# Optimization experiments

Hardware: AMD Instinct MI355X
Metric: run time of the kernel (lower is better)

The kernel has to match this reference:

```python
import jax, jax.numpy as jnp
import numpy as np
from jax import lax

NX, NY = 6, 6
NB = NX * NY            # 36 blocks
B, S = 64, 256          # batch, sample_count
EPS = 1e-6

def build_edges(nx, ny):
    edges = []
    for i in range(nx):
        for j in range(ny):
            for dx, dy in [(-1, 0), (0, -1), (0, 1), (1, 0)]:
                x, y = i + dx, j + dy
                if 0 <= x < nx and 0 <= y < ny:
                    edges.append((j * nx + i, y * nx + x))
    return np.array(edges, np.int32)   # (120, 2)

EDGES_NP = build_edges(NX, NY)
NE = len(EDGES_NP)  # 120

def setup_inputs() -> dict:
    key = jax.random.key(0)
    ks = jax.random.split(key, 24)
    f32 = jnp.float32
    d = {
        "image":      jax.random.normal(ks[0], (B, 1, 32, 32), f32),
        "edge_noise": jax.random.uniform(ks[1], (B, S, NE), f32),
        "u_s":        jax.random.uniform(ks[2], (B, S, NB), f32),
        "u_d":        jax.random.uniform(ks[3], (B, S, NB), f32),
        # CNN params (OIHW)
        "cw1": jax.random.normal(ks[4], (32, 1, 5, 5), f32) * 0.05,
        "cb1": jnp.zeros((32,), f32),
        "cw2": jax.random.normal(ks[5], (32, 32, 5, 5), f32) * 0.05,
        "cb2": jnp.zeros((32,), f32),
        "cw3": jax.random.normal(ks[6], (64, 32, 5, 5), f32) * 0.05,
        "cb3": jnp.zeros((64,), f32),
        "cw4": jax.random.normal(ks[7], (64, 64, 5, 5), f32) * 0.05,
        "cb4": jnp.zeros((64,), f32),
        # is_connected MLP
        "wc1": jax.random.normal(ks[8], (256, 256), f32) * 0.05,
        "bc1": jnp.zeros((256,), f32),
        "wc2": jax.random.normal(ks[9], (256, NE), f32) * 0.05,
        "bc2": jnp.zeros((NE,), f32),
        # is_endpoint MLP
        "we1": jax.random.normal(ks[10], (256, 256), f32) * 0.05,
        "be1": jnp.zeros((256,), f32),
        "we2": jax.random.normal(ks[11], (256, NB), f32) * 0.05,
        "be2": jnp.zeros((NB,), f32),
        "edges": jnp.asarray(EDGES_NP),  # (NE, 2) int32, constants
    }
    return d

def _conv(x, w, b):
    y = lax.conv_general_dilated(x, w, (1, 1), 'VALID',
                                 dimension_numbers=('NCHW', 'OIHW', 'NCHW'))
    return y + b[None, :, None, None]

def _pool2(x):
    return lax.reduce_window(x, -jnp.inf, lax.max, (1, 1, 2, 2), (1, 1, 2, 2), 'VALID')

def reference(image, edge_noise, u_s, u_d,
              cw1, cb1, cw2, cb2, cw3, cb3, cw4, cb4,
              wc1, bc1, wc2, bc2, we1, be1, we2, be2, edges):
    # ---- CNN feature extractor ----
    h = _conv(image, cw1, cb1)
    h = _conv(h, cw2, cb2)
    h = _pool2(h)
    h = _conv(h, cw3, cb3)
    h = _conv(h, cw4, cb4)
    h = _pool2(h)
    emb = h.reshape(h.shape[0], -1)              # (B, 256)

    # ---- heads ----
    p_conn = jax.nn.sigmoid(jax.nn.relu(emb @ wc1 + bc1) @ wc2 + bc2)   # (B, NE)
    p_ep   = jax.nn.sigmoid(jax.nn.relu(emb @ we1 + be1) @ we2 + be2)   # (B, NB)

    pc = jnp.clip(p_conn, EPS, 1.0 - EPS)
    pe = jnp.clip(p_ep, EPS, 1.0 - EPS)
    cat = pe / pe.sum(-1, keepdims=True)
    logcat = jnp.log(cat)                        # (B, NB)

    # ---- Monte-Carlo sampling (ISED blackbox) ----
    conn = (edge_noise < pc[:, None, :]).astype(pc.dtype)               # (B,S,NE) Bernoulli
    g_s = -jnp.log(-jnp.log(jnp.clip(u_s, EPS, 1.0 - EPS)))
    g_d = -jnp.log(-jnp.log(jnp.clip(u_d, EPS, 1.0 - EPS)))
    s_idx = jnp.argmax(logcat[:, None, :] + g_s, axis=-1)               # (B,S) categorical
    d_idx = jnp.argmax(logcat[:, None, :] + g_d, axis=-1)               # (B,S)

    # ---- batched BFS reachability via boolean matrix squaring ----
    oh_u = jax.nn.one_hot(edges[:, 0], NB, dtype=pc.dtype)              # (NE, NB)
    oh_v = jax.nn.one_hot(edges[:, 1], NB, dtype=pc.dtype)
    e_sym = jnp.einsum('eu,ev->euv', oh_u, oh_v) + jnp.einsum('eu,ev->evu', oh_u, oh_v)
    A = jnp.minimum(jnp.einsum('bse,euv->bsuv', conn, e_sym), 1.0)      # (B,S,36,36)

    R = jnp.minimum(A + jnp.eye(NB, dtype=A.dtype), 1.0)
    for _ in range(6):                           # (I+A)^(2^6), covers path len<=36
        R = jnp.minimum(R @ R, 1.0)
    P = jnp.minimum(A @ R, 1.0)                  # paths of length >= 1 (BFS semantics)

    Pv = jnp.take_along_axis(P, s_idx[:, :, None, None], axis=2)[:, :, 0, :]  # (B,S,36)
    exists = (jnp.take_along_axis(Pv, d_idx[:, :, None], axis=2)[:, :, 0] > 0.5).astype(pc.dtype)  # (B,S)

    # ---- sample-probability weighting (differentiable ISED estimator) ----
    logw = (conn * jnp.log(pc)[:, None, :] + (1.0 - conn) * jnp.log1p(-pc)[:, None, :]).sum(-1)
    logw = logw + jnp.take_along_axis(logcat, s_idx, axis=1) \
                + jnp.take_along_axis(logcat, d_idx, axis=1)            # (B,S)
    w = jax.nn.softmax(logw, axis=1)
    p1 = (w * exists).sum(axis=1)                # P(path exists)
    return jnp.stack([1.0 - p1, p1], axis=-1)    # (B, 2)
```

## Files before the change

### kernel.cpp

```cpp
#include <hip/hip_runtime.h>

typedef unsigned long long u64;
#define EPSF 1e-6f

__global__ __launch_bounds__(1024, 4) void k_conv2(const float* __restrict__ img,
                                                   const float* __restrict__ cw1,
                                                   const float* __restrict__ cb1,
                                                   const float* __restrict__ cw2,
                                                   const float* __restrict__ cb2,
                                                   float* __restrict__ p1w) {
  int ocq = blockIdx.x, b = blockIdx.y;
  __shared__ float smem[33440];
  float* w2s = smem + 25984;
  float* simg = smem + 32384;
  int t = threadIdx.x;
  if (t < 1024) {
    int y = t >> 5, x = t & 31;
    simg[y * 33 + x] = img[b * 1024 + t];
  }
  {
    const float4* src = (const float4*)(cw2 + ocq * 8 * 800);
    for (int k4 = t; k4 < 1600; k4 += 1024) {
      float4 v = src[k4];
      float vv[4] = {v.x, v.y, v.z, v.w};
      int k = k4 * 4;
#pragma unroll
      for (int r = 0; r < 4; ++r) {
        int kk = k + r;
        int o = kk / 800, rest = kk % 800;
        w2s[rest * 8 + o] = vv[r];
      }
    }
  }
  __syncthreads();
  if (t < 896) {
    int ic = t / 28, x = t % 28;
    float w1[25];
#pragma unroll
    for (int k = 0; k < 25; ++k) w1[k] = cw1[ic * 25 + k];
    float bias = cb1[ic];
    float acc[5];
#pragma unroll
    for (int k = 0; k < 5; ++k) acc[k] = bias;
    float* orow = smem + ic * 812 + x;
#pragma unroll
    for (int rr = 0; rr < 32; ++rr) {
      float in[5];
#pragma unroll
      for (int c = 0; c < 5; ++c) in[c] = simg[rr * 33 + x + c];
#pragma unroll
      for (int ky = 0; ky < 5; ++ky) {
        if (rr < ky || rr - ky > 27) continue;
        int slot = (rr - ky) % 5;
#pragma unroll
        for (int kx = 0; kx < 5; ++kx)
          acc[slot] = fmaf(w1[ky * 5 + kx], in[kx], acc[slot]);
      }
      if (rr >= 4) {
        int slot = (rr - 4) % 5;
        orow[(rr - 4) * 29] = acc[slot];
        acc[slot] = bias;
      }
    }
  }
  int w = __builtin_amdgcn_readfirstlane(t >> 6);
  int ocg = w & 1;
  int icq = w >> 1;
  int l = t & 63;
  int py = l >> 3, px = l & 7;
  int oc0 = ocq * 8 + ocg * 4;
  float acc[4][9];
#pragma unroll
  for (int o = 0; o < 4; ++o)
#pragma unroll
    for (int e = 0; e < 9; ++e) acc[o][e] = 0.f;
  __syncthreads();

  const float* base0 = smem + icq * 4 * 812 + (3 * py) * 29 + 3 * px;
  const float* wk0 = w2s + icq * 800 + ocg * 4;
#pragma unroll
  for (int icl = 0; icl < 4; ++icl) {
    const float* base = base0 + icl * 812;
    float win[7][7];
#pragma unroll
    for (int rr = 0; rr < 7; ++rr)
#pragma unroll
      for (int m = 0; m < 7; ++m) win[rr][m] = base[rr * 29 + m];
    const float* wk = wk0 + icl * 200;
#pragma unroll
    for (int ky = 0; ky < 5; ++ky) {
      float wq[5][4];
#pragma unroll
      for (int kx = 0; kx < 5; ++kx)
        *(float4*)wq[kx] = *(const float4*)(wk + (ky * 5 + kx) * 8);
#pragma unroll
      for (int i = 0; i < 3; ++i) {
#pragma unroll
        for (int kx = 0; kx < 5; ++kx) {
#pragma unroll
          for (int jj = 0; jj < 3; ++jj) {
            float v = win[i + ky][jj + kx];
            acc[0][i * 3 + jj] = fmaf(wq[kx][0], v, acc[0][i * 3 + jj]);
            acc[1][i * 3 + jj] = fmaf(wq[kx][1], v, acc[1][i * 3 + jj]);
            acc[2][i * 3 + jj] = fmaf(wq[kx][2], v, acc[2][i * 3 + jj]);
            acc[3][i * 3 + jj] = fmaf(wq[kx][3], v, acc[3][i * 3 + jj]);
          }
        }
      }
    }
  }

  __syncthreads();
  float* slots = smem;
  float* cbuf = smem + 18432;
  int chunk = ocg * 2304 + l * 9;
  if (icq >= 4) {
    float* d = slots + (icq - 4) * 4608 + chunk;
#pragma unroll
    for (int o = 0; o < 4; ++o)
#pragma unroll
      for (int e = 0; e < 9; ++e) d[o * 576 + e] = acc[o][e];
  }
  __syncthreads();
  if (icq < 4) {
    const float* s = slots + icq * 4608 + chunk;
#pragma unroll
    for (int o = 0; o < 4; ++o)
#pragma unroll
      for (int e = 0; e < 9; ++e) acc[o][e] += s[o * 576 + e];
  }
  __syncthreads();
  if (icq == 2 || icq == 3) {
    float* d = slots + (icq - 2) * 4608 + chunk;
#pragma unroll
    for (int o = 0; o < 4; ++o)
#pragma unroll
      for (int e = 0; e < 9; ++e) d[o * 576 + e] = acc[o][e];
  }
  __syncthreads();
  if (icq < 2) {
    const float* s = slots + icq * 4608 + chunk;
#pragma unroll
    for (int o = 0; o < 4; ++o)
#pragma unroll
      for (int e = 0; e < 9; ++e) acc[o][e] += s[o * 576 + e];
  }
  __syncthreads();
  if (icq == 1) {
    float* d = slots + chunk;
#pragma unroll
    for (int o = 0; o < 4; ++o)
#pragma unroll
      for (int e = 0; e < 9; ++e) d[o * 576 + e] = acc[o][e];
  }
  __syncthreads();
  if (icq == 0) {
    const float* s = slots + chunk;
#pragma unroll
    for (int o = 0; o < 4; ++o) {
      float bias = cb2[oc0 + o];
#pragma unroll
      for (int i = 0; i < 3; ++i)
#pragma unroll
        for (int jj = 0; jj < 3; ++jj)
          cbuf[(ocg * 4 + o) * 576 + (3 * py + i) * 24 + 3 * px + jj] =
              acc[o][i * 3 + jj] + s[o * 576 + i * 3 + jj] + bias;
    }
  }
  __syncthreads();
  for (int k = t; k < 1152; k += 1024) {
    int o = k / 144, rem = k % 144;
    int PY = rem / 12, PX = rem % 12;
    const float* b0 = cbuf + o * 576 + (2 * PY) * 24 + 2 * PX;
    float m = fmaxf(fmaxf(b0[0], b0[1]), fmaxf(b0[24], b0[25]));
    p1w[((size_t)b * 32 + ocq * 8 + o) * 144 + PY * 12 + PX] = m;
  }
}

__global__ __launch_bounds__(256) void k_conv3(const float* __restrict__ p1w,
                                               const float* __restrict__ cw3,
                                               const float* __restrict__ cb3,
                                               float* __restrict__ c3) {
  int oc8 = blockIdx.x, b = blockIdx.y;
  __shared__ float smem[11008];
  float* w3s = smem;
  float* ins = smem + 6400;
  int t = threadIdx.x;
  {
    const float4* src = (const float4*)(p1w + b * 32 * 144);
    float4* dst = (float4*)ins;
    for (int k = t; k < 1152; k += 256) dst[k] = src[k];
  }
  {
    const float4* src = (const float4*)(cw3 + oc8 * 8 * 800);
    for (int k4 = t; k4 < 1600; k4 += 256) {
      float4 v = src[k4];
      float vv[4] = {v.x, v.y, v.z, v.w};
      int k = k4 * 4;
#pragma unroll
      for (int r = 0; r < 4; ++r) {
        int kk = k + r;
        int o = kk / 800, rest = kk % 800;
        w3s[rest * 8 + o] = vv[r];
      }
    }
  }
  int g = t >> 4, p = t & 15;
  int ocg = p >> 3, row = p & 7;
  float acc[4][8];
#pragma unroll
  for (int j = 0; j < 4; ++j)
#pragma unroll
    for (int c = 0; c < 8; ++c) acc[j][c] = 0.f;
  __syncthreads();
#pragma unroll
  for (int icl = 0; icl < 2; ++icl) {
    int ic = g + icl * 16;
#pragma unroll
    for (int ky = 0; ky < 5; ++ky) {
      const float4* rp = (const float4*)(ins + ic * 144 + (row + ky) * 12);
      float win[12];
#pragma unroll
      for (int q = 0; q < 3; ++q) {
        float4 v = rp[q];
        win[4 * q] = v.x; win[4 * q + 1] = v.y; win[4 * q + 2] = v.z; win[4 * q + 3] = v.w;
      }
      const float* wb = w3s + (ic * 25 + ky * 5) * 8 + ocg * 4;
#pragma unroll
      for (int kx = 0; kx < 5; ++kx) {
        float wq[4];
        *(float4*)wq = *(const float4*)(wb + kx * 8);
#pragma unroll
        for (int c = 0; c < 8; ++c) {
#pragma unroll
          for (int j = 0; j < 4; ++j) acc[j][c] = fmaf(wq[j], win[c + kx], acc[j][c]);
        }
      }
    }
  }
  float* buf = smem;
  __syncthreads();
  if (g >= 8) {
    float* d = buf + (g - 8) * 512 + p * 32;
#pragma unroll
    for (int j = 0; j < 4; ++j)
#pragma unroll
      for (int c = 0; c < 8; ++c) d[j * 8 + c] = acc[j][c];
  }
  __syncthreads();
  if (g < 8) {
    const float* s = buf + g * 512 + p * 32;
#pragma unroll
    for (int j = 0; j < 4; ++j)
#pragma unroll
      for (int c = 0; c < 8; ++c) acc[j][c] += s[j * 8 + c];
  }
  __syncthreads();
  if (g >= 4 && g < 8) {
    float* d = buf + (g - 4) * 512 + p * 32;
#pragma unroll
    for (int j = 0; j < 4; ++j)
#pragma unroll
      for (int c = 0; c < 8; ++c) d[j * 8 + c] = acc[j][c];
  }
  __syncthreads();
  if (g < 4) {
    const float* s = buf + g * 512 + p * 32;
#pragma unroll
    for (int j = 0; j < 4; ++j)
#pragma unroll
      for (int c = 0; c < 8; ++c) acc[j][c] += s[j * 8 + c];
  }
  __syncthreads();
  if (g == 2 || g == 3) {
    float* d = buf + (g - 2) * 512 + p * 32;
#pragma unroll
    for (int j = 0; j < 4; ++j)
#pragma unroll
      for (int c = 0; c < 8; ++c) d[j * 8 + c] = acc[j][c];
  }
  __syncthreads();
  if (g < 2) {
    const float* s = buf + g * 512 + p * 32;
#pragma unroll
    for (int j = 0; j < 4; ++j)
#pragma unroll
      for (int c = 0; c < 8; ++c) acc[j][c] += s[j * 8 + c];
  }
  __syncthreads();
  if (g == 1) {
    float* d = buf + p * 32;
#pragma unroll
    for (int j = 0; j < 4; ++j)
#pragma unroll
      for (int c = 0; c < 8; ++c) d[j * 8 + c] = acc[j][c];
  }
  __syncthreads();
  if (g == 0) {
    const float* s = buf + p * 32;
#pragma unroll
    for (int j = 0; j < 4; ++j) {
      float bias = cb3[oc8 * 8 + ocg * 4 + j];
      float4 v0, v1;
      v0.x = acc[j][0] + s[j * 8 + 0] + bias; v0.y = acc[j][1] + s[j * 8 + 1] + bias;
      v0.z = acc[j][2] + s[j * 8 + 2] + bias; v0.w = acc[j][3] + s[j * 8 + 3] + bias;
      v1.x = acc[j][4] + s[j * 8 + 4] + bias; v1.y = acc[j][5] + s[j * 8 + 5] + bias;
      v1.z = acc[j][6] + s[j * 8 + 6] + bias; v1.w = acc[j][7] + s[j * 8 + 7] + bias;
      float* op = c3 + (b * 64 + oc8 * 8 + ocg * 4 + j) * 64 + row * 8;
      *(float4*)op = v0; *(float4*)(op + 4) = v1;
    }
  }
}

__global__ __launch_bounds__(256) void k_conv4(const float* __restrict__ c3,
                                               const float* __restrict__ cw4,
                                               const float* __restrict__ cb4,
                                               float* __restrict__ emb) {
  int oc8 = blockIdx.x, b = blockIdx.y;
  __shared__ float smem[17152];
  float* w4s = smem;
  float* ins = smem + 12800;
  int t = threadIdx.x;
  {
    const float4* src = (const float4*)(c3 + b * 4096);
    for (int k = t; k < 1024; k += 256) {
      int ic = k >> 4, q = k & 15;
      *(float4*)(ins + ic * 68 + q * 4) = src[k];
    }
  }
  {
    const float4* src = (const float4*)(cw4 + oc8 * 8 * 1600);
    for (int k4 = t; k4 < 3200; k4 += 256) {
      float4 v = src[k4];
      float vv[4] = {v.x, v.y, v.z, v.w};
      int k = k4 * 4;
#pragma unroll
      for (int r = 0; r < 4; ++r) {
        int kk = k + r;
        int o = kk / 1600, rest = kk % 1600;
        w4s[rest * 8 + o] = vv[r];
      }
    }
  }
  int g = t >> 3, p = t & 7;
  int ocg = p >> 2, row = p & 3;
  float acc[4][4];
#pragma unroll
  for (int j = 0; j < 4; ++j)
#pragma unroll
    for (int c = 0; c < 4; ++c) acc[j][c] = 0.f;
  __syncthreads();
#pragma unroll
  for (int icl = 0; icl < 2; ++icl) {
    int ic = g + icl * 32;
#pragma unroll
    for (int ky = 0; ky < 5; ++ky) {
      const float4* rp = (const float4*)(ins + ic * 68 + (row + ky) * 8);
      float win[8];
#pragma unroll
      for (int q = 0; q < 2; ++q) {
        float4 v = rp[q];
        win[4 * q] = v.x; win[4 * q + 1] = v.y; win[4 * q + 2] = v.z; win[4 * q + 3] = v.w;
      }
      const float* wb = w4s + (ic * 25 + ky * 5) * 8 + ocg * 4;
#pragma unroll
      for (int kx = 0; kx < 5; ++kx) {
        float wq[4];
        *(float4*)wq = *(const float4*)(wb + kx * 8);
#pragma unroll
        for (int c = 0; c < 4; ++c) {
#pragma unroll
          for (int j = 0; j < 4; ++j) acc[j][c] = fmaf(wq[j], win[c + kx], acc[j][c]);
        }
      }
    }
  }
  float* buf = smem;
#pragma unroll
  for (int half = 16; half >= 1; half >>= 1) {
    __syncthreads();
    if (g >= half && g < 2 * half) {
      float* d = buf + (g - half) * 128 + p * 16;
#pragma unroll
      for (int j = 0; j < 4; ++j)
#pragma unroll
        for (int c = 0; c < 4; ++c) d[j * 4 + c] = acc[j][c];
    }
    __syncthreads();
    if (g < half) {
      const float* s = buf + g * 128 + p * 16;
#pragma unroll
      for (int j = 0; j < 4; ++j)
#pragma unroll
        for (int c = 0; c < 4; ++c) acc[j][c] += s[j * 4 + c];
    }
  }
  float* pb = buf + 2048;
  if (g == 0) {
#pragma unroll
    for (int j = 0; j < 4; ++j) {
      float bias = cb4[oc8 * 8 + ocg * 4 + j];
#pragma unroll
      for (int c = 0; c < 4; ++c) pb[(ocg * 4 + j) * 16 + row * 4 + c] = acc[j][c] + bias;
    }
  }
  __syncthreads();
  if (t < 32) {
    int o = t >> 2, q = t & 3, py = q >> 1, px = q & 1;
    const float* b0 = pb + o * 16 + (2 * py) * 4 + 2 * px;
    float m = fmaxf(fmaxf(b0[0], b0[1]), fmaxf(b0[4], b0[5]));
    emb[b * 256 + (oc8 * 8 + o) * 4 + py * 2 + px] = m;
  }
}

__global__ __launch_bounds__(256) void k_tail(const float* __restrict__ emb,
    const float* __restrict__ wc1, const float* __restrict__ bc1,
    const float* __restrict__ wc2, const float* __restrict__ bc2,
    const float* __restrict__ we1, const float* __restrict__ be1,
    const float* __restrict__ we2, const float* __restrict__ be2,
    const float* __restrict__ enoise, const float* __restrict__ us,
    const float* __restrict__ ud, const int* __restrict__ edges,
    float* __restrict__ out) {
  int b = blockIdx.x, t = threadIdx.x;
  __shared__ float e_s[256], h_s[256];
  __shared__ __align__(16) float pc_s[120];
  __shared__ __align__(16) float lpc_s[120];
  __shared__ __align__(16) float l1m_s[120];
  __shared__ __align__(16) float lcat_s[36];
  __shared__ __align__(16) int einfo[120];
  __shared__ float red_s[256];
  __shared__ float aux;
  e_s[t] = emb[b * 256 + t];
  if (t < 120) {
    int u = edges[2 * t], v = edges[2 * t + 1];
    int d = v - u;
    int isV = (d == 6 || d == -6) ? 1 : 0;
    int pos = d > 0 ? u : v;
    einfo[t] = pos | (isV << 6);
  }
  __syncthreads();
  {
    float s = bc1[t];
    for (int i = 0; i < 256; i += 4) {
      s = fmaf(e_s[i], wc1[i * 256 + t], s);
      s = fmaf(e_s[i + 1], wc1[(i + 1) * 256 + t], s);
      s = fmaf(e_s[i + 2], wc1[(i + 2) * 256 + t], s);
      s = fmaf(e_s[i + 3], wc1[(i + 3) * 256 + t], s);
    }
    h_s[t] = fmaxf(s, 0.f);
  }
  __syncthreads();
  if (t < 120) {
    float s2 = bc2[t];
    for (int i = 0; i < 256; ++i) s2 = fmaf(h_s[i], wc2[i * 120 + t], s2);
    float p = 1.f / (1.f + expf(-s2));
    p = fminf(fmaxf(p, EPSF), 1.f - EPSF);
    pc_s[t] = p;
    lpc_s[t] = logf(p);
    l1m_s[t] = log1pf(-p);
  }
  __syncthreads();
  {
    float s = be1[t];
    for (int i = 0; i < 256; i += 4) {
      s = fmaf(e_s[i], we1[i * 256 + t], s);
      s = fmaf(e_s[i + 1], we1[(i + 1) * 256 + t], s);
      s = fmaf(e_s[i + 2], we1[(i + 2) * 256 + t], s);
      s = fmaf(e_s[i + 3], we1[(i + 3) * 256 + t], s);
    }
    h_s[t] = fmaxf(s, 0.f);
  }
  __syncthreads();
  if (t < 36) {
    float s2 = be2[t];
    for (int i = 0; i < 256; ++i) s2 = fmaf(h_s[i], we2[i * 36 + t], s2);
    float p = 1.f / (1.f + expf(-s2));
    p = fminf(fmaxf(p, EPSF), 1.f - EPSF);
    red_s[t] = p;
  }
  __syncthreads();
  if (t == 0) {
    float sm = 0.f;
    for (int j = 0; j < 36; ++j) sm += red_s[j];
    aux = sm;
  }
  __syncthreads();
  if (t < 36) lcat_s[t] = logf(red_s[t] / aux);
  __syncthreads();

  float logw = 0.f;
  u64 H = 0, V = 0;
  {
    const float4* np = (const float4*)(enoise + ((size_t)(b * 256 + t)) * 120);
#pragma unroll
    for (int q = 0; q < 30; ++q) {
      float4 nz = np[q];
      float4 p4 = ((const float4*)pc_s)[q];
      float4 lp4 = ((const float4*)lpc_s)[q];
      float4 lm4 = ((const float4*)l1m_s)[q];
      int4 e4 = ((const int4*)einfo)[q];
      float nv[4] = {nz.x, nz.y, nz.z, nz.w};
      float pv[4] = {p4.x, p4.y, p4.z, p4.w};
      float lv[4] = {lp4.x, lp4.y, lp4.z, lp4.w};
      float mv[4] = {lm4.x, lm4.y, lm4.z, lm4.w};
      int ev[4] = {e4.x, e4.y, e4.z, e4.w};
#pragma unroll
      for (int r = 0; r < 4; ++r) {
        bool conn = nv[r] < pv[r];
        logw += conn ? lv[r] : mv[r];
        if (conn) {
          u64 bit = 1ull << (ev[r] & 63);
          if (ev[r] & 64) V |= bit; else H |= bit;
        }
      }
    }
  }
  int si = 0, di = 0;
  {
    const float4* up = (const float4*)(us + ((size_t)(b * 256 + t)) * 36);
    float best = -1e30f;
#pragma unroll
    for (int q = 0; q < 9; ++q) {
      float4 uv = up[q];
      float4 lc4 = ((const float4*)lcat_s)[q];
      float vv[4] = {uv.x, uv.y, uv.z, uv.w};
      float lc[4] = {lc4.x, lc4.y, lc4.z, lc4.w};
#pragma unroll
      for (int r = 0; r < 4; ++r) {
        float u = fminf(fmaxf(vv[r], EPSF), 1.f - EPSF);
        float gq = -logf(-logf(u));
        float val = lc[r] + gq;
        if (val > best) { best = val; si = q * 4 + r; }
      }
    }
  }
  {
    const float4* up = (const float4*)(ud + ((size_t)(b * 256 + t)) * 36);
    float best = -1e30f;
#pragma unroll
    for (int q = 0; q < 9; ++q) {
      float4 uv = up[q];
      float4 lc4 = ((const float4*)lcat_s)[q];
      float vv[4] = {uv.x, uv.y, uv.z, uv.w};
      float lc[4] = {lc4.x, lc4.y, lc4.z, lc4.w};
#pragma unroll
      for (int r = 0; r < 4; ++r) {
        float u = fminf(fmaxf(vv[r], EPSF), 1.f - EPSF);
        float gq = -logf(-logf(u));
        float val = lc[r] + gq;
        if (val > best) { best = val; di = q * 4 + r; }
      }
    }
  }
  logw += lcat_s[si] + lcat_s[di];

  u64 comp = 1ull << si;
  while (true) {
    u64 prev = comp;
    comp |= ((comp & H) << 1) | ((comp >> 1) & H);
    comp |= ((comp & V) << 6) | ((comp >> 6) & V);
    if (comp == prev) break;
  }
  float ex;
  if (si == di) ex = (comp != (1ull << si)) ? 1.f : 0.f;
  else ex = ((comp >> di) & 1ull) ? 1.f : 0.f;

  __syncthreads();
  red_s[t] = logw; __syncthreads();
  for (int off = 128; off > 0; off >>= 1) {
    if (t < off) red_s[t] = fmaxf(red_s[t], red_s[t + off]);
    __syncthreads();
  }
  float m = red_s[0]; __syncthreads();
  float evx = expf(logw - m);
  red_s[t] = evx; __syncthreads();
  for (int off = 128; off > 0; off >>= 1) {
    if (t < off) red_s[t] += red_s[t + off];
    __syncthreads();
  }
  float den = red_s[0]; __syncthreads();
  red_s[t] = evx * ex; __syncthreads();
  for (int off = 128; off > 0; off >>= 1) {
    if (t < off) red_s[t] += red_s[t + off];
    __syncthreads();
  }
  if (t == 0) {
    float p1v = red_s[0] / den;
    out[b * 2] = 1.f - p1v;
    out[b * 2 + 1] = p1v;
  }
}

extern "C" void kernel_launch(void* const* d_in, const int* in_sizes, int n_in,
                              void* d_out, int out_size, void* d_ws, size_t ws_size,
                              hipStream_t stream) {
  const float* image = (const float*)d_in[0];
  const float* enoise = (const float*)d_in[1];
  const float* us = (const float*)d_in[2];
  const float* udn = (const float*)d_in[3];
  const float* cw1 = (const float*)d_in[4];
  const float* cb1 = (const float*)d_in[5];
  const float* cw2 = (const float*)d_in[6];
  const float* cb2 = (const float*)d_in[7];
  const float* cw3 = (const float*)d_in[8];
  const float* cb3 = (const float*)d_in[9];
  const float* cw4 = (const float*)d_in[10];
  const float* cb4 = (const float*)d_in[11];
  const float* wc1 = (const float*)d_in[12];
  const float* bc1 = (const float*)d_in[13];
  const float* wc2 = (const float*)d_in[14];
  const float* bc2 = (const float*)d_in[15];
  const float* we1 = (const float*)d_in[16];
  const float* be1 = (const float*)d_in[17];
  const float* we2 = (const float*)d_in[18];
  const float* be2 = (const float*)d_in[19];
  const int* edges = (const int*)d_in[20];

  float* ws = (float*)d_ws;
  float* p1w = ws;
  float* c3 = ws + 294912;
  float* emb = ws + 557056;
  float* outp = (float*)d_out;

  k_conv2<<<dim3(4, 64), dim3(1024), 0, stream>>>(image, cw1, cb1, cw2, cb2, p1w);
  k_conv3<<<dim3(8, 64), dim3(256), 0, stream>>>(p1w, cw3, cb3, c3);
  k_conv4<<<dim3(8, 64), dim3(256), 0, stream>>>(c3, cw4, cb4, emb);
  k_tail<<<dim3(64), dim3(256), 0, stream>>>(emb, wc1, bc1, wc2, bc2,
                                             we1, be1, we2, be2,
                                             enoise, us, udn, edges, outp);
}
```

Measured before the change: 130.4 us.

## Split sampling tail across 4 blocks per batch with staged smem loads and finalize kernel

The tail kernel is split so each batch row runs on 4 blocks, each handling 64 samples. Noise and uniform inputs are loaded coalesced into padded shared memory, and the per-sample work runs on one wavefront that reduces with shuffles instead of block-wide shared-memory reductions. Partial max, sum and hit values are combined by a new small kernel using log-sum-exp rescaling. The trade-off is that each of the 4 blocks recomputes the two MLPs, only 64 of 256 threads do the sampling work, and there is one more kernel launch.

```diff
diff --git a/kernel.cpp b/kernel.cpp
--- a/kernel.cpp
+++ b/kernel.cpp
@@ -413,22 +413,24 @@
   }
 }
 
-__global__ __launch_bounds__(256) void k_tail(const float* __restrict__ emb,
+__global__ __launch_bounds__(256) void k_hmc(const float* __restrict__ emb,
     const float* __restrict__ wc1, const float* __restrict__ bc1,
     const float* __restrict__ wc2, const float* __restrict__ bc2,
     const float* __restrict__ we1, const float* __restrict__ be1,
     const float* __restrict__ we2, const float* __restrict__ be2,
     const float* __restrict__ enoise, const float* __restrict__ us,
     const float* __restrict__ ud, const int* __restrict__ edges,
-    float* __restrict__ out) {
-  int b = blockIdx.x, t = threadIdx.x;
-  __shared__ float e_s[256], h_s[256];
+    float* __restrict__ part3) {
+  int chunk = blockIdx.x, b = blockIdx.y, t = threadIdx.x;
+  __shared__ __align__(16) float en_s[64 * 124];
+  __shared__ __align__(16) float us_s[64 * 40];
+  __shared__ __align__(16) float ud_s[64 * 40];
+  __shared__ float e_s[256], h_s[256], pe_s[36];
   __shared__ __align__(16) float pc_s[120];
   __shared__ __align__(16) float lpc_s[120];
   __shared__ __align__(16) float l1m_s[120];
   __shared__ __align__(16) float lcat_s[36];
   __shared__ __align__(16) int einfo[120];
-  __shared__ float red_s[256];
   __shared__ float aux;
   e_s[t] = emb[b * 256 + t];
   if (t < 120) {
@@ -438,6 +440,25 @@
     int pos = d > 0 ? u : v;
     einfo[t] = pos | (isV << 6);
   }
+  {
+    const float4* src = (const float4*)(enoise + ((size_t)(b * 256 + chunk * 64)) * 120);
+    for (int k = t; k < 1920; k += 256) {
+      float4 v = src[k];
+      int s = k / 30, e4 = k % 30;
+      *(float4*)(en_s + s * 124 + e4 * 4) = v;
+    }
+  }
+  {
+    const float4* srcA = (const float4*)(us + ((size_t)(b * 256 + chunk * 64)) * 36);
+    const float4* srcB = (const float4*)(ud + ((size_t)(b * 256 + chunk * 64)) * 36);
+    for (int k = t; k < 576; k += 256) {
+      float4 va = srcA[k];
+      float4 vb = srcB[k];
+      int s = k / 9, e4 = k % 9;
+      *(float4*)(us_s + s * 40 + e4 * 4) = va;
+      *(float4*)(ud_s + s * 40 + e4 * 4) = vb;
+    }
+  }
   __syncthreads();
   {
     float s = bc1[t];
@@ -476,119 +497,127 @@
     for (int i = 0; i < 256; ++i) s2 = fmaf(h_s[i], we2[i * 36 + t], s2);
     float p = 1.f / (1.f + expf(-s2));
     p = fminf(fmaxf(p, EPSF), 1.f - EPSF);
-    red_s[t] = p;
+    pe_s[t] = p;
   }
   __syncthreads();
   if (t == 0) {
     float sm = 0.f;
-    for (int j = 0; j < 36; ++j) sm += red_s[j];
+    for (int j = 0; j < 36; ++j) sm += pe_s[j];
     aux = sm;
   }
   __syncthreads();
-  if (t < 36) lcat_s[t] = logf(red_s[t] / aux);
-  __syncthreads();
-
-  float logw = 0.f;
-  u64 H = 0, V = 0;
-  {
-    const float4* np = (const float4*)(enoise + ((size_t)(b * 256 + t)) * 120);
-#pragma unroll
-    for (int q = 0; q < 30; ++q) {
-      float4 nz = np[q];
-      float4 p4 = ((const float4*)pc_s)[q];
-      float4 lp4 = ((const float4*)lpc_s)[q];
-      float4 lm4 = ((const float4*)l1m_s)[q];
-      int4 e4 = ((const int4*)einfo)[q];
-      float nv[4] = {nz.x, nz.y, nz.z, nz.w};
-      float pv[4] = {p4.x, p4.y, p4.z, p4.w};
-      float lv[4] = {lp4.x, lp4.y, lp4.z, lp4.w};
-      float mv[4] = {lm4.x, lm4.y, lm4.z, lm4.w};
-      int ev[4] = {e4.x, e4.y, e4.z, e4.w};
-#pragma unroll
-      for (int r = 0; r < 4; ++r) {
-        bool conn = nv[r] < pv[r];
-        logw += conn ? lv[r] : mv[r];
-        if (conn) {
-          u64 bit = 1ull << (ev[r] & 63);
-          if (ev[r] & 64) V |= bit; else H |= bit;
+  if (t < 36) lcat_s[t] = logf(pe_s[t] / aux);
+  __syncthreads();
+
+  if (t < 64) {
+    float logw = 0.f;
+    u64 H = 0, V = 0;
+    {
+      const float4* np = (const float4*)(en_s + t * 124);
+#pragma unroll
+      for (int q = 0; q < 30; ++q) {
+        float4 nz = np[q];
+        float4 p4 = ((const float4*)pc_s)[q];
+        float4 lp4 = ((const float4*)lpc_s)[q];
+        float4 lm4 = ((const float4*)l1m_s)[q];
+        int4 e4 = ((const int4*)einfo)[q];
+        float nv[4] = {nz.x, nz.y, nz.z, nz.w};
+        float pv[4] = {p4.x, p4.y, p4.z, p4.w};
+        float lv[4] = {lp4.x, lp4.y, lp4.z, lp4.w};
+        float mv[4] = {lm4.x, lm4.y, lm4.z, lm4.w};
+        int ev[4] = {e4.x, e4.y, e4.z, e4.w};
+#pragma unroll
+        for (int r = 0; r < 4; ++r) {
+          bool conn = nv[r] < pv[r];
+          logw += conn ? lv[r] : mv[r];
+          if (conn) {
+            u64 bit = 1ull << (ev[r] & 63);
+            if (ev[r] & 64) V |= bit; else H |= bit;
+          }
         }
       }
     }
-  }
-  int si = 0, di = 0;
-  {
-    const float4* up = (const float4*)(us + ((size_t)(b * 256 + t)) * 36);
-    float best = -1e30f;
-#pragma unroll
-    for (int q = 0; q < 9; ++q) {
-      float4 uv = up[q];
-      float4 lc4 = ((const float4*)lcat_s)[q];
-      float vv[4] = {uv.x, uv.y, uv.z, uv.w};
-      float lc[4] = {lc4.x, lc4.y, lc4.z, lc4.w};
-#pragma unroll
-      for (int r = 0; r < 4; ++r) {
-        float u = fminf(fmaxf(vv[r], EPSF), 1.f - EPSF);
-        float gq = -logf(-logf(u));
-        float val = lc[r] + gq;
-        if (val > best) { best = val; si = q * 4 + r; }
-      }
-    }
-  }
-  {
-    const float4* up = (const float4*)(ud + ((size_t)(b * 256 + t)) * 36);
-    float best = -1e30f;
-#pragma unroll
-    for (int q = 0; q < 9; ++q) {
-      float4 uv = up[q];
-      float4 lc4 = ((const float4*)lcat_s)[q];
-      float vv[4] = {uv.x, uv.y, uv.z, uv.w};
-      float lc[4] = {lc4.x, lc4.y, lc4.z, lc4.w};
-#pragma unroll
-      for (int r = 0; r < 4; ++r) {
-        float u = fminf(fmaxf(vv[r], EPSF), 1.f - EPSF);
-        float gq = -logf(-logf(u));
-        float val = lc[r] + gq;
-        if (val > best) { best = val; di = q * 4 + r; }
-      }
-    }
-  }
-  logw += lcat_s[si] + lcat_s[di];
-
-  u64 comp = 1ull << si;
-  while (true) {
-    u64 prev = comp;
-    comp |= ((comp & H) << 1) | ((comp >> 1) & H);
-    comp |= ((comp & V) << 6) | ((comp >> 6) & V);
-    if (comp == prev) break;
-  }
-  float ex;
-  if (si == di) ex = (comp != (1ull << si)) ? 1.f : 0.f;
-  else ex = ((comp >> di) & 1ull) ? 1.f : 0.f;
-
-  __syncthreads();
-  red_s[t] = logw; __syncthreads();
-  for (int off = 128; off > 0; off >>= 1) {
-    if (t < off) red_s[t] = fmaxf(red_s[t], red_s[t + off]);
-    __syncthreads();
-  }
-  float m = red_s[0]; __syncthreads();
-  float evx = expf(logw - m);
-  red_s[t] = evx; __syncthreads();
-  for (int off = 128; off > 0; off >>= 1) {
-    if (t < off) red_s[t] += red_s[t + off];
-    __syncthreads();
-  }
-  float den = red_s[0]; __syncthreads();
-  red_s[t] = evx * ex; __syncthreads();
-  for (int off = 128; off > 0; off >>= 1) {
-    if (t < off) red_s[t] += red_s[t + off];
-    __syncthreads();
-  }
-  if (t == 0) {
-    float p1v = red_s[0] / den;
-    out[b * 2] = 1.f - p1v;
-    out[b * 2 + 1] = p1v;
-  }
+    int si = 0, di = 0;
+    {
+      const float4* up = (const float4*)(us_s + t * 40);
+      float best = -1e30f;
+#pragma unroll
+      for (int q = 0; q < 9; ++q) {
+        float4 uv = up[q];
+        float4 lc4 = ((const float4*)lcat_s)[q];
+        float vv[4] = {uv.x, uv.y, uv.z, uv.w};
+        float lc[4] = {lc4.x, lc4.y, lc4.z, lc4.w};
+#pragma unroll
+        for (int r = 0; r < 4; ++r) {
+          float u = fminf(fmaxf(vv[r], EPSF), 1.f - EPSF);
+          float gq = -logf(-logf(u));
+          float val = lc[r] + gq;
+          if (val > best) { best = val; si = q * 4 + r; }
+        }
+      }
+    }
+    {
+      const float4* up = (const float4*)(ud_s + t * 40);
+      float best = -1e30f;
+#pragma unroll
+      for (int q = 0; q < 9; ++q) {
+        float4 uv = up[q];
+        float4 lc4 = ((const float4*)lcat_s)[q];
+        float vv[4] = {uv.x, uv.y, uv.z, uv.w};
+        float lc[4] = {lc4.x, lc4.y, lc4.z, lc4.w};
+#pragma unroll
+        for (int r = 0; r < 4; ++r) {
+          float u = fminf(fmaxf(vv[r], EPSF), 1.f - EPSF);
+          float gq = -logf(-logf(u));
+          float val = lc[r] + gq;
+          if (val > best) { best = val; di = q * 4 + r; }
+        }
+      }
+    }
+    logw += lcat_s[si] + lcat_s[di];
+
+    u64 comp = 1ull << si;
+    while (true) {
+      u64 prev = comp;
+      comp |= ((comp & H) << 1) | ((comp >> 1) & H);
+      comp |= ((comp & V) << 6) | ((comp >> 6) & V);
+      if (comp == prev) break;
+    }
+    float ex;
+    if (si == di) ex = (comp != (1ull << si)) ? 1.f : 0.f;
+    else ex = ((comp >> di) & 1ull) ? 1.f : 0.f;
+
+    float m = logw;
+#pragma unroll
+    for (int off = 1; off < 64; off <<= 1) m = fmaxf(m, __shfl_xor(m, off));
+    float ev = expf(logw - m);
+    float sm = ev;
+#pragma unroll
+    for (int off = 1; off < 64; off <<= 1) sm += __shfl_xor(sm, off);
+    float hit = ev * ex;
+#pragma unroll
+    for (int off = 1; off < 64; off <<= 1) hit += __shfl_xor(hit, off);
+    if (t == 0) {
+      float* d = part3 + (size_t)(b * 4 + chunk) * 3;
+      d[0] = m; d[1] = sm; d[2] = hit;
+    }
+  }
+}
+
+__global__ __launch_bounds__(64) void k_fin(const float* __restrict__ part3,
+                                            float* __restrict__ out) {
+  int b = threadIdx.x;
+  float m0 = part3[(b * 4 + 0) * 3], s0 = part3[(b * 4 + 0) * 3 + 1], h0 = part3[(b * 4 + 0) * 3 + 2];
+  float m1 = part3[(b * 4 + 1) * 3], s1 = part3[(b * 4 + 1) * 3 + 1], h1 = part3[(b * 4 + 1) * 3 + 2];
+  float m2 = part3[(b * 4 + 2) * 3], s2 = part3[(b * 4 + 2) * 3 + 1], h2 = part3[(b * 4 + 2) * 3 + 2];
+  float m3 = part3[(b * 4 + 3) * 3], s3 = part3[(b * 4 + 3) * 3 + 1], h3 = part3[(b * 4 + 3) * 3 + 2];
+  float M = fmaxf(fmaxf(m0, m1), fmaxf(m2, m3));
+  float e0 = expf(m0 - M), e1 = expf(m1 - M), e2 = expf(m2 - M), e3 = expf(m3 - M);
+  float den = s0 * e0 + s1 * e1 + s2 * e2 + s3 * e3;
+  float num = h0 * e0 + h1 * e1 + h2 * e2 + h3 * e3;
+  float p1v = num / den;
+  out[b * 2] = 1.f - p1v;
+  out[b * 2 + 1] = p1v;
 }
 
 extern "C" void kernel_launch(void* const* d_in, const int* in_sizes, int n_in,
@@ -620,12 +649,14 @@
   float* p1w = ws;
   float* c3 = ws + 294912;
   float* emb = ws + 557056;
+  float* part3 = ws + 573440;
   float* outp = (float*)d_out;
 
   k_conv2<<<dim3(4, 64), dim3(1024), 0, stream>>>(image, cw1, cb1, cw2, cb2, p1w);
   k_conv3<<<dim3(8, 64), dim3(256), 0, stream>>>(p1w, cw3, cb3, c3);
   k_conv4<<<dim3(8, 64), dim3(256), 0, stream>>>(c3, cw4, cb4, emb);
-  k_tail<<<dim3(64), dim3(256), 0, stream>>>(emb, wc1, bc1, wc2, bc2,
-                                             we1, be1, we2, be2,
-                                             enoise, us, udn, edges, outp);
+  k_hmc<<<dim3(4, 64), dim3(256), 0, stream>>>(emb, wc1, bc1, wc2, bc2,
+                                               we1, be1, we2, be2,
+                                               enoise, us, udn, edges, part3);
+  k_fin<<<dim3(1), dim3(64), 0, stream>>>(part3, outp);
 }
```

New measurement: 129.3 us. Within noise of the previous version (-0.8%).
